# Performance work log

Measured on AMD Instinct MI355X. Metric: run time of the kernel, lower is better.

## Reference

```python
import jax, jax.numpy as jnp
import numpy as np

LOG_2PI = float(np.log(2.0 * np.pi))


def setup_inputs() -> dict:
    key = jax.random.key(0)
    k1, k2, k3, k4 = jax.random.split(key, 4)
    B, Tin, Tout, D = 32, 512, 2048, 256
    memory = jax.random.normal(k1, (B, Tin, D), dtype=jnp.float32)
    # durations in [1, 7) frames per token (mean ~4 -> ~Tout total frames)
    duration = jax.random.uniform(k2, (B, Tin), dtype=jnp.float32) * 6.0 + 1.0
    # positive Gaussian widths in [0.5, 2.0)
    sigma = jax.random.uniform(k3, (B, Tin), dtype=jnp.float32) * 1.5 + 0.5
    output_lengths = jnp.full((B,), Tout, dtype=jnp.int32)
    mask = jax.random.uniform(k4, (B, Tin)) < 0.1
    return {"memory": memory, "duration": duration, "sigma": sigma,
            "output_lengths": output_lengths, "mask": mask}


def reference(memory, duration, sigma, output_lengths, mask):
    # memory: (B,Tin,D); duration,sigma,mask: (B,Tin); output_lengths: (B,)
    Tout = int(np.max(np.asarray(output_lengths)))
    frames = jnp.arange(Tout, dtype=jnp.float32)[None, None, :]          # (1,1,Tout)
    center = jnp.cumsum(duration, axis=-1) - 0.5 * duration              # (B,Tin)
    c = center[..., None]                                                # (B,Tin,1)
    s = sigma[..., None]                                                 # (B,Tin,1)
    # Normal(loc=c, scale=s).log_prob(frames).exp()
    z = (frames - c) / s
    alignment = jnp.exp(-0.5 * z * z - jnp.log(s) - 0.5 * LOG_2PI)       # (B,Tin,Tout)
    alignment = jnp.where(mask[..., None], 0.0, alignment)               # masked_fill
    attn_weights = alignment / (jnp.sum(alignment, axis=1, keepdims=True) + 1e-8)
    # bmm(attn^T, memory): (B,Tout,Tin) @ (B,Tin,D) -> (B,Tout,D)
    upsampled = jnp.einsum('bit,bid->btd', attn_weights, memory)
    return upsampled, attn_weights
```

## Files before the change

kernel.cpp:

```cpp
#include <hip/hip_runtime.h>
#include <hip/hip_bf16.h>
#include <math.h>

#define HALF_LOG_2PI 0.9189385332046727f
#define WIN 32.0f
#define TILE_T 16

typedef float f32x4 __attribute__((ext_vector_type(4)));

__global__ void prep_k(const float* __restrict__ duration,
                       const float* __restrict__ sigma,
                       const void* __restrict__ mask,
                       float* __restrict__ center,
                       float* __restrict__ amp,
                       float* __restrict__ inv_sigma,
                       int B, int Tin) {
    __shared__ float s[1024];
    __shared__ int s_not[2];
    int b = blockIdx.x, i = threadIdx.x;
    if (i < 2) s_not[i] = 0;
    __syncthreads();
    {
        const unsigned int* mw = (const unsigned int*)mask;
        int nwords = (B * Tin) >> 2;
        int nI = 0, nF = 0;
        for (int k = i; k < nwords; k += blockDim.x) {
            unsigned int w = mw[k];
            nI |= (w != 0u && w != 1u);
            nF |= (w != 0u && w != 0x3F800000u);
        }
        if (nI) atomicOr(&s_not[0], 1);
        if (nF) atomicOr(&s_not[1], 1);
    }
    size_t gi = (size_t)b * Tin + i;
    float d = duration[gi];
    s[i] = d;
    __syncthreads();
    for (int off = 1; off < Tin; off <<= 1) {
        float v = (i >= off) ? s[i - off] : 0.0f;
        __syncthreads();
        s[i] += v;
        __syncthreads();
    }
    float c = s[i] - 0.5f * d;
    int mode = s_not[0] ? (s_not[1] ? 2 : 1) : 0;
    bool m;
    if (mode == 0)      m = ((const int*)mask)[gi] != 0;
    else if (mode == 1) m = ((const float*)mask)[gi] != 0.0f;
    else                m = ((const unsigned char*)mask)[gi] != 0;
    float sg = sigma[gi];
    center[gi]    = c;
    inv_sigma[gi] = 1.0f / sg;
    amp[gi]       = m ? 0.0f : __expf(-__logf(sg) - HALF_LOG_2PI);
}

__global__ __launch_bounds__(256) void denom_k(
        const float* __restrict__ center, const float* __restrict__ amp,
        const float* __restrict__ inv_sigma,
        float* __restrict__ inv_den, int* __restrict__ lo_out,
        int* __restrict__ cnt_out, int Tin, int Tout) {
    __shared__ float sc[1024], sa[1024], si[1024];
    int b = blockIdx.y;
    int t = blockIdx.x * 256 + threadIdx.x;
    for (int i = threadIdx.x; i < Tin; i += 256) {
        size_t g = (size_t)b * Tin + i;
        sc[i] = center[g]; sa[i] = amp[g]; si[i] = inv_sigma[g];
    }
    __syncthreads();
    if (t >= Tout) return;
    float tf = (float)t;
    int lo = 0, hi = Tin;
    while (lo < hi) {
        int mid = (lo + hi) >> 1;
        if (sc[mid] < tf - WIN) lo = mid + 1; else hi = mid;
    }
    float sum = 0.0f;
    int i = lo;
    for (; i < Tin; ++i) {
        float cc = sc[i];
        if (cc > tf + WIN) break;
        float z = (tf - cc) * si[i];
        sum += sa[i] * __expf(-0.5f * z * z);
    }
    size_t g = (size_t)b * Tout + t;
    inv_den[g]  = 1.0f / (sum + 1e-8f);
    lo_out[g]   = lo;
    cnt_out[g]  = i - lo;
}

__global__ __launch_bounds__(256) void attn_k(
        const float* __restrict__ center, const float* __restrict__ amp,
        const float* __restrict__ inv_sigma, const float* __restrict__ inv_den,
        float* __restrict__ attn, int Tin, int Tout) {
    int bi = blockIdx.x;
    int b  = bi / Tin;
    float c = center[bi], a = amp[bi], inv = inv_sigma[bi];
    const float* iden = inv_den + (size_t)b * Tout;
    float* row = attn + (size_t)bi * Tout;
    for (int t4 = threadIdx.x * 4; t4 < Tout; t4 += 256 * 4) {
        f32x4 rv;
        if ((float)(t4 + 3) < c - WIN || (float)t4 > c + WIN) {
            rv = (f32x4)0.0f;
        } else {
            #pragma unroll
            for (int j = 0; j < 4; ++j) {
                float dlt = (float)(t4 + j) - c;
                if (fabsf(dlt) < WIN) {
                    float z = dlt * inv;
                    rv[j] = a * __expf(-0.5f * z * z) * iden[t4 + j];
                } else rv[j] = 0.0f;
            }
        }
        __builtin_nontemporal_store(rv, (f32x4*)(row + t4));
    }
}

__global__ __launch_bounds__(256) void upsample_k(
        const float* __restrict__ mem, const float* __restrict__ center,
        const float* __restrict__ amp, const float* __restrict__ inv_sigma,
        const float* __restrict__ inv_den, const int* __restrict__ lo_ws,
        const int* __restrict__ cnt_ws, float* __restrict__ out,
        int Tin, int Tout, int D) {
    __shared__ __align__(16) float w_s[TILE_T][128];
    __shared__ float s_iden[TILE_T];
    __shared__ int s_lo, s_cnt;
    int nwg = gridDim.x;
    int wid = blockIdx.x;
    int work = wid;
    if ((nwg & 7) == 0) {
        int chunk = nwg >> 3;
        work = (wid & 7) * chunk + (wid >> 3);
    }
    int tpb = Tout / TILE_T;
    int b   = work / tpb;
    int t0  = (work - b * tpb) * TILE_T;
    int tid = threadIdx.x;
    if (tid == 0) {
        size_t g0 = (size_t)b * Tout + t0;
        size_t g1 = g0 + (TILE_T - 1);
        int lo0 = lo_ws[g0];
        int cnt = lo_ws[g1] + cnt_ws[g1] - lo0;
        s_lo  = lo0;
        s_cnt = cnt > 128 ? 128 : cnt;
    }
    if (tid < TILE_T) s_iden[tid] = inv_den[(size_t)b * Tout + t0 + tid];
    __syncthreads();
    int lo0 = s_lo, wcnt = s_cnt;
    #pragma unroll
    for (int rep = 0; rep < (TILE_T * 128) / 256; ++rep) {
        int id = tid + rep * 256;
        int f = id >> 7, w = id & 127;
        float wgt = 0.0f;
        int i = lo0 + w;
        if (w < wcnt && i < Tin) {
            size_t gi = (size_t)b * Tin + i;
            float dlt = (float)(t0 + f) - center[gi];
            if (fabsf(dlt) < WIN) {
                float z = dlt * inv_sigma[gi];
                wgt = amp[gi] * __expf(-0.5f * z * z) * s_iden[f];
            }
        }
        w_s[f][w] = wgt;
    }
    __syncthreads();
    for (int d = tid; d < D; d += 256) {
        float acc[TILE_T];
        #pragma unroll
        for (int f = 0; f < TILE_T; ++f) acc[f] = 0.0f;
        const float* mrow = mem + ((size_t)b * Tin + lo0) * D + d;
        int w4 = wcnt & ~3;
        for (int w = 0; w < w4; w += 4) {
            float m0 = mrow[(size_t)(w + 0) * D];
            float m1 = mrow[(size_t)(w + 1) * D];
            float m2 = mrow[(size_t)(w + 2) * D];
            float m3 = mrow[(size_t)(w + 3) * D];
            #pragma unroll
            for (int f = 0; f < TILE_T; ++f) {
                f32x4 wv = *(const f32x4*)&w_s[f][w];
                acc[f] += wv.x * m0 + wv.y * m1 + wv.z * m2 + wv.w * m3;
            }
        }
        for (int w = w4; w < wcnt; ++w) {
            float m0 = mrow[(size_t)w * D];
            #pragma unroll
            for (int f = 0; f < TILE_T; ++f) acc[f] += w_s[f][w] * m0;
        }
        float* orow = out + ((size_t)b * Tout + t0) * D + d;
        #pragma unroll
        for (int f = 0; f < TILE_T; ++f)
            __builtin_nontemporal_store(acc[f], orow + (size_t)f * D);
    }
}

extern "C" void kernel_launch(void* const* d_in, const int* in_sizes, int n_in,
                              void* d_out, int out_size, void* d_ws, size_t ws_size,
                              hipStream_t stream) {
    const float* memory   = (const float*)d_in[0];
    const float* duration = (const float*)d_in[1];
    const float* sigma    = (const float*)d_in[2];
    const void*  mask     = d_in[4];

    int B    = in_sizes[3];
    int Tin  = in_sizes[1] / B;
    int D    = in_sizes[0] / (B * Tin);
    int Tout = out_size / (B * (D + Tin));

    float* out_up   = (float*)d_out;
    float* out_attn = out_up + (size_t)B * Tout * D;

    float* center = (float*)d_ws;
    float* amp    = center + (size_t)B * Tin;
    float* inv    = amp    + (size_t)B * Tin;
    float* iden   = inv    + (size_t)B * Tin;
    int*   lo     = (int*)(iden + (size_t)B * Tout);
    int*   cnt    = lo + (size_t)B * Tout;

    prep_k<<<B, Tin, 0, stream>>>(duration, sigma, mask,
                                  center, amp, inv, B, Tin);
    denom_k<<<dim3((Tout + 255) / 256, B), 256, 0, stream>>>(
        center, amp, inv, iden, lo, cnt, Tin, Tout);
    attn_k<<<B * Tin, 256, 0, stream>>>(center, amp, inv, iden,
                                        out_attn, Tin, Tout);
    upsample_k<<<(B * Tout) / TILE_T, 256, 0, stream>>>(
        memory, center, amp, inv, iden, lo, cnt, out_up, Tin, Tout, D);
}
```

Measured before the change: 62.69 us.

## Use bf16 MFMA for upsample matmul with transposed memory tile in LDS

Replaces the scalar FP32 FMA loop in upsample_k with MFMA 16x16x32 bf16 instructions. The memory window is converted to bf16 and stored transposed in shared memory, and the weights are converted to bf16 fragments. The window is capped at 96 instead of 128 and the mapping is hardwired to D=256. This lowers output precision to bf16 inputs and drops the i<Tin bounds check, which risks reading out of bounds and a mismatch with the reference tolerance.

```diff
diff --git a/kernel.cpp b/kernel.cpp
--- a/kernel.cpp
+++ b/kernel.cpp
@@ -5,8 +5,12 @@
 #define HALF_LOG_2PI 0.9189385332046727f
 #define WIN 32.0f
 #define TILE_T 16
+#define KPAD 96
+#define MROWPAD 104
+#define WROWPAD 108
 
 typedef float f32x4 __attribute__((ext_vector_type(4)));
+typedef short bf16x8 __attribute__((ext_vector_type(8)));
 
 __global__ void prep_k(const float* __restrict__ duration,
                        const float* __restrict__ sigma,
@@ -121,7 +125,8 @@
         const float* __restrict__ inv_den, const int* __restrict__ lo_ws,
         const int* __restrict__ cnt_ws, float* __restrict__ out,
         int Tin, int Tout, int D) {
-    __shared__ __align__(16) float w_s[TILE_T][128];
+    __shared__ __align__(16) float w_s[TILE_T][WROWPAD];
+    __shared__ __align__(16) unsigned short sMT[256][MROWPAD];
     __shared__ float s_iden[TILE_T];
     __shared__ int s_lo, s_cnt;
     int nwg = gridDim.x;
@@ -141,19 +146,17 @@
         int lo0 = lo_ws[g0];
         int cnt = lo_ws[g1] + cnt_ws[g1] - lo0;
         s_lo  = lo0;
-        s_cnt = cnt > 128 ? 128 : cnt;
+        s_cnt = cnt > KPAD ? KPAD : cnt;
     }
     if (tid < TILE_T) s_iden[tid] = inv_den[(size_t)b * Tout + t0 + tid];
     __syncthreads();
     int lo0 = s_lo, wcnt = s_cnt;
-    #pragma unroll
-    for (int rep = 0; rep < (TILE_T * 128) / 256; ++rep) {
-        int id = tid + rep * 256;
-        int f = id >> 7, w = id & 127;
+
+    for (int id = tid; id < TILE_T * KPAD; id += 256) {
+        int f = id / KPAD, w = id - f * KPAD;
         float wgt = 0.0f;
-        int i = lo0 + w;
-        if (w < wcnt && i < Tin) {
-            size_t gi = (size_t)b * Tin + i;
+        if (w < wcnt) {
+            size_t gi = (size_t)b * Tin + lo0 + w;
             float dlt = (float)(t0 + f) - center[gi];
             if (fabsf(dlt) < WIN) {
                 float z = dlt * inv_sigma[gi];
@@ -162,33 +165,53 @@
         }
         w_s[f][w] = wgt;
     }
-    __syncthreads();
-    for (int d = tid; d < D; d += 256) {
-        float acc[TILE_T];
+    {
+        const float* mcol = mem + ((size_t)b * Tin + lo0) * D + tid;
+        #pragma unroll 4
+        for (int r = 0; r < KPAD; r += 2) {
+            float m0 = (r     < wcnt) ? mcol[(size_t)r * D]       : 0.0f;
+            float m1 = (r + 1 < wcnt) ? mcol[(size_t)(r + 1) * D] : 0.0f;
+            __hip_bfloat162 h2 = __float22bfloat162_rn(make_float2(m0, m1));
+            *(unsigned*)&sMT[tid][r] = *(unsigned*)&h2;
+        }
+    }
+    __syncthreads();
+
+    int lane = tid & 63, wave = tid >> 6;
+    int m16 = lane & 15, kg = lane >> 4;
+    bf16x8 afr[3];
+    #pragma unroll
+    for (int s = 0; s < 3; ++s) {
+        int k0 = s * 32 + kg * 8;
+        f32x4 a0 = *(const f32x4*)&w_s[m16][k0];
+        f32x4 a1 = *(const f32x4*)&w_s[m16][k0 + 4];
+        __hip_bfloat162 p0 = __float22bfloat162_rn(make_float2(a0.x, a0.y));
+        __hip_bfloat162 p1 = __float22bfloat162_rn(make_float2(a0.z, a0.w));
+        __hip_bfloat162 p2 = __float22bfloat162_rn(make_float2(a1.x, a1.y));
+        __hip_bfloat162 p3 = __float22bfloat162_rn(make_float2(a1.z, a1.w));
+        union { bf16x8 v; unsigned u[4]; } au;
+        au.u[0] = *(unsigned*)&p0; au.u[1] = *(unsigned*)&p1;
+        au.u[2] = *(unsigned*)&p2; au.u[3] = *(unsigned*)&p3;
+        afr[s] = au.v;
+    }
+    #pragma unroll
+    for (int q = 0; q < 4; ++q) {
+        int nb = wave * 64 + q * 16;
+        f32x4 acc = {0.0f, 0.0f, 0.0f, 0.0f};
         #pragma unroll
-        for (int f = 0; f < TILE_T; ++f) acc[f] = 0.0f;
-        const float* mrow = mem + ((size_t)b * Tin + lo0) * D + d;
-        int w4 = wcnt & ~3;
-        for (int w = 0; w < w4; w += 4) {
-            float m0 = mrow[(size_t)(w + 0) * D];
-            float m1 = mrow[(size_t)(w + 1) * D];
-            float m2 = mrow[(size_t)(w + 2) * D];
-            float m3 = mrow[(size_t)(w + 3) * D];
-            #pragma unroll
-            for (int f = 0; f < TILE_T; ++f) {
-                f32x4 wv = *(const f32x4*)&w_s[f][w];
-                acc[f] += wv.x * m0 + wv.y * m1 + wv.z * m2 + wv.w * m3;
-            }
-        }
-        for (int w = w4; w < wcnt; ++w) {
-            float m0 = mrow[(size_t)w * D];
-            #pragma unroll
-            for (int f = 0; f < TILE_T; ++f) acc[f] += w_s[f][w] * m0;
-        }
-        float* orow = out + ((size_t)b * Tout + t0) * D + d;
+        for (int s = 0; s < 3; ++s) {
+            int k0 = s * 32 + kg * 8;
+            bf16x8 bfr = *(const bf16x8*)&sMT[nb + m16][k0];
+            acc = __builtin_amdgcn_mfma_f32_16x16x32_bf16(afr[s], bfr, acc,
+                                                          0, 0, 0);
+        }
+        int n = nb + m16;
         #pragma unroll
-        for (int f = 0; f < TILE_T; ++f)
-            __builtin_nontemporal_store(acc[f], orow + (size_t)f * D);
+        for (int r = 0; r < 4; ++r) {
+            int m = kg * 4 + r;
+            __builtin_nontemporal_store(
+                acc[r], out + ((size_t)(b * Tout + t0 + m)) * D + n);
+        }
     }
 }
 
```

Result: slower. 92.47 us (+47.5%).
